# Optimization experiments

Hardware: AMD Instinct MI355X
Metric: run time of the kernel (lower is better)

The kernel has to match this reference:

```python
import jax, jax.numpy as jnp
import numpy as np

N = 100000   # nodes
E = 1600000  # edges
S = 4        # state_dimension
H = 64       # hidden_channels


def _gcn_conv(x, row, col, W, b):
    """PyG GCNConv: h = x @ W; add self-loops; symmetric deg^-1/2 norm; scatter-add; + bias."""
    n = x.shape[0]
    h = x @ W  # [N, out]
    loop = jnp.arange(n, dtype=row.dtype)
    r = jnp.concatenate([row, loop])  # sources (with self-loops)
    c = jnp.concatenate([col, loop])  # targets (with self-loops)
    deg = jax.ops.segment_sum(jnp.ones(r.shape[0], h.dtype), c, num_segments=n)
    dinv = jnp.where(deg > 0, jax.lax.rsqrt(deg), 0.0)
    norm = dinv[r] * dinv[c]                      # [E+N]
    msg = h[r] * norm[:, None]                    # gather + scale, [E+N, out]
    out = jax.ops.segment_sum(msg, c, num_segments=n)  # scatter-add
    return out + b


def setup_inputs() -> dict:
    key = jax.random.key(0)
    k1, k2, k3, k4 = jax.random.split(key, 4)
    x = jax.random.normal(k1, (N, S), dtype=jnp.float32)
    edge_index = jax.random.randint(k2, (2, E), 0, N, dtype=jnp.int32)
    # Glorot-ish init for the two GCNConv linear layers (+ zero bias, PyG default)
    W1 = jax.random.normal(k3, (S, H), dtype=jnp.float32) * (1.0 / np.sqrt(S))
    b1 = jnp.zeros((H,), jnp.float32)
    W2 = jax.random.normal(k4, (H, S), dtype=jnp.float32) * (1.0 / np.sqrt(H))
    b2 = jnp.zeros((S,), jnp.float32)
    return {"x": x, "edge_index": edge_index, "W1": W1, "b1": b1, "W2": W2, "b2": b2}


def reference(x, edge_index, W1, b1, W2, b2):
    row, col = edge_index[0], edge_index[1]
    h = _gcn_conv(x, row, col, W1, b1)
    h = jax.nn.relu(h)
    out = _gcn_conv(h, row, col, W2, b2)
    return out
```

## Files before the change

### kernel.cpp

```cpp
#include <hip/hip_runtime.h>


#define CSHIFT  10
#define CNODES  1024
#define EPB     4096
#define PTH     512
#define PERBLK  96
#define CAPC    18432
#define HCAP    9216
#define ANODES  128
#define ACAP    2432

__global__ void __launch_bounds__(PTH) k_part(
        const int* __restrict__ row, const int* __restrict__ col,
        int e, int Kc, int NB, int* __restrict__ cnt,
        unsigned* __restrict__ stripe) {
    __shared__ int cur[128];
    int t = threadIdx.x, bx = blockIdx.x;
    if (t < 128) cur[t] = 0;
    __syncthreads();
    int lo = bx * EPB;
    int cbuf[8], rbuf[8];
#pragma unroll
    for (int k = 0; k < 8; ++k) {
        int i = lo + t + k * PTH;
        if (i < e) { cbuf[k] = col[i]; rbuf[k] = row[i]; }
        else { cbuf[k] = -1; rbuf[k] = 0; }
    }
    size_t sbase = (size_t)bx * PERBLK;
    size_t bstride = (size_t)NB * PERBLK;
#pragma unroll
    for (int k = 0; k < 8; ++k) {
        int c = cbuf[k];
        if (c < 0) continue;
        int b = c >> CSHIFT;
        int j = atomicAdd(&cur[b], 1);
        if (j < PERBLK)
            stripe[(size_t)b * bstride + sbase + j] =
                ((unsigned)rbuf[k] << CSHIFT) | (unsigned)(c & (CNODES - 1));
    }
    __syncthreads();
    if (t < Kc) cnt[t * NB + bx] = min(cur[t], PERBLK);
}

__global__ void __launch_bounds__(1024) k_sortH(
        const int* __restrict__ cnt, const unsigned* __restrict__ stripe,
        unsigned* __restrict__ sortedg, int* __restrict__ rstart,
        int* __restrict__ mtot, const float4* __restrict__ x,
        float* __restrict__ dinv, float4* __restrict__ y, int n, int NB) {
    __shared__ int hist[CNODES];
    __shared__ int cur[512];
    __shared__ int cntl[512];
    __shared__ unsigned sorted[HCAP];
    __shared__ int wsum[16], wpre[16];
    __shared__ int lowsh, msh;
    int bh = blockIdx.x, b = bh >> 1, h = bh & 1;
    int t = threadIdx.x, lane = t & 63, wv = t >> 6;
    for (int i = t; i < NB; i += 1024) cntl[i] = cnt[b * NB + i];
    hist[t] = 0;
    __syncthreads();
    size_t s0 = (size_t)b * NB * PERBLK;
    int nslot4 = (NB * PERBLK) >> 2;
    const uint4* st4 = (const uint4*)(stripe + s0);
    for (int g = t; g < nslot4; g += 1024) {
        int slot = g << 2;
        int seg = slot / PERBLK;
        int j = slot - seg * PERBLK;
        int cb = cntl[seg];
        if (j >= cb) continue;
        uint4 w = st4[g];
        atomicAdd(&hist[w.x & (CNODES - 1)], 1);
        if (j + 1 < cb) atomicAdd(&hist[w.y & (CNODES - 1)], 1);
        if (j + 2 < cb) atomicAdd(&hist[w.z & (CNODES - 1)], 1);
        if (j + 3 < cb) atomicAdd(&hist[w.w & (CNODES - 1)], 1);
    }
    __syncthreads();
    int hv = hist[t];
    int v = hv;
#pragma unroll
    for (int off = 1; off < 64; off <<= 1) {
        int u = __shfl_up(v, off);
        if (lane >= off) v += u;
    }
    if (lane == 63) wsum[wv] = v;
    __syncthreads();
    if (t < 16) {
        int s = 0;
        for (int i = 0; i < t; ++i) s += wsum[i];
        wpre[t] = s;
    }
    __syncthreads();
    int incl = v + wpre[wv];
    if (t == 511) lowsh = incl;
    if (t == 1023) msh = incl;
    __syncthreads();
    int st = incl - hv;
    int low = lowsh, m = msh;
    int base = h ? low : 0;
    if ((t >> 9) == h) {
        cur[t & 511] = st - base;
        rstart[(b << CSHIFT) + t] = b * CAPC + st;
        int node = (b << CSHIFT) + t;
        if (node < n) {
            float di = rsqrtf((float)hv + 1.0f);
            dinv[node] = di;
            float4 xv = x[node];
            y[node] = make_float4(xv.x * di, xv.y * di, xv.z * di, xv.w * di);
        }
    }
    if (t == 0 && h == 0) mtot[b] = m;
    __syncthreads();
    for (int g = t; g < nslot4; g += 1024) {
        int slot = g << 2;
        int seg = slot / PERBLK;
        int j = slot - seg * PERBLK;
        int cb = cntl[seg];
        if (j >= cb) continue;
        uint4 w = st4[g];
        int l0 = w.x & (CNODES - 1);
        if ((l0 >> 9) == h) { int p = atomicAdd(&cur[l0 & 511], 1); if (p < HCAP) sorted[p] = w.x >> CSHIFT; }
        if (j + 1 < cb) { int l = w.y & (CNODES - 1);
            if ((l >> 9) == h) { int p = atomicAdd(&cur[l & 511], 1); if (p < HCAP) sorted[p] = w.y >> CSHIFT; } }
        if (j + 2 < cb) { int l = w.z & (CNODES - 1);
            if ((l >> 9) == h) { int p = atomicAdd(&cur[l & 511], 1); if (p < HCAP) sorted[p] = w.z >> CSHIFT; } }
        if (j + 3 < cb) { int l = w.w & (CNODES - 1);
            if ((l >> 9) == h) { int p = atomicAdd(&cur[l & 511], 1); if (p < HCAP) sorted[p] = w.w >> CSHIFT; } }
    }
    __syncthreads();
    int cown = h ? (m - low) : low;
    int wb = min(cown, HCAP);
    size_t d0 = (size_t)b * CAPC + base;
    for (int i = t; i < wb; i += 1024) sortedg[d0 + i] = sorted[i];
}

__global__ void __launch_bounds__(512) k_mid(
        const unsigned* __restrict__ ere, const int* __restrict__ rstart,
        const int* __restrict__ mtot, const float* __restrict__ dinv,
        const float4* __restrict__ x, const float4* __restrict__ y,
        const float* __restrict__ W1, const float* __restrict__ b1,
        const float* __restrict__ W2, const float* __restrict__ b2,
        float4* __restrict__ z, float4* __restrict__ out, int n) {
    __shared__ unsigned recs[ACAP];
    __shared__ float4 sums[ANODES];
    int g = blockIdx.x, t = threadIdx.x;
    int nlo = g * ANODES;
    int b = nlo >> CSHIFT;
    int s0 = rstart[nlo];
    int e0 = ((g & 7) == 7) ? b * CAPC + min(mtot[b], CAPC)
                            : rstart[nlo + ANODES];
    int len = min(e0 - s0, ACAP);
    for (int i = t; i < len; i += 512) recs[i] = ere[s0 + i];
    __syncthreads();
    int tt = t >> 2, q = t & 3;
    int s = rstart[nlo + tt] - s0;
    int epos = (tt == ANODES - 1) ? len : min(rstart[nlo + tt + 1] - s0, len);
    float vx = 0.f, vy = 0.f, vz = 0.f, vw = 0.f;
    int i = s + q;
    while (i + 12 < epos) {
        int r0 = recs[i], r1 = recs[i + 4], r2 = recs[i + 8], r3 = recs[i + 12];
        float4 a0 = y[r0], a1 = y[r1], a2 = y[r2], a3 = y[r3];
        vx += a0.x + a1.x + a2.x + a3.x;
        vy += a0.y + a1.y + a2.y + a3.y;
        vz += a0.z + a1.z + a2.z + a3.z;
        vw += a0.w + a1.w + a2.w + a3.w;
        i += 16;
    }
    for (; i < epos; i += 4) {
        float4 a = y[recs[i]];
        vx += a.x; vy += a.y; vz += a.z; vw += a.w;
    }
    vx += __shfl_xor(vx, 1); vx += __shfl_xor(vx, 2);
    vy += __shfl_xor(vy, 1); vy += __shfl_xor(vy, 2);
    vz += __shfl_xor(vz, 1); vz += __shfl_xor(vz, 2);
    vw += __shfl_xor(vw, 1); vw += __shfl_xor(vw, 2);
    if (q == 0) sums[tt] = make_float4(vx, vy, vz, vw);
    __syncthreads();
    int node = nlo + t;
    if (t < ANODES && node < n) {
        float di = dinv[node], sl = di * di;
        float4 sv = sums[t];
        float4 xv = x[node];
        float a0 = di * sv.x + xv.x * sl;
        float a1 = di * sv.y + xv.y * sl;
        float a2 = di * sv.z + xv.z * sl;
        float a3 = di * sv.w + xv.w * sl;
        float t0 = 0.f, t1 = 0.f, t2 = 0.f, t3 = 0.f;
#pragma unroll 8
        for (int j = 0; j < 64; ++j) {
            float hh = b1[j] + a0 * W1[j] + a1 * W1[64 + j] + a2 * W1[128 + j] + a3 * W1[192 + j];
            hh = fmaxf(hh, 0.f);
            t0 += hh * W2[j * 4 + 0];
            t1 += hh * W2[j * 4 + 1];
            t2 += hh * W2[j * 4 + 2];
            t3 += hh * W2[j * 4 + 3];
        }
        z[node] = make_float4(t0 * di, t1 * di, t2 * di, t3 * di);
        out[node] = make_float4(b2[0] + t0 * sl, b2[1] + t1 * sl,
                                b2[2] + t2 * sl, b2[3] + t3 * sl);
    }
}

__global__ void __launch_bounds__(512) k_acc2(
        const unsigned* __restrict__ ere, const int* __restrict__ rstart,
        const int* __restrict__ mtot, const float* __restrict__ dinv,
        const float4* __restrict__ z, float4* __restrict__ out, int n) {
    __shared__ unsigned recs[ACAP];
    __shared__ float4 sums[ANODES];
    int g = blockIdx.x, t = threadIdx.x;
    int nlo = g * ANODES;
    int b = nlo >> CSHIFT;
    int s0 = rstart[nlo];
    int e0 = ((g & 7) == 7) ? b * CAPC + min(mtot[b], CAPC)
                            : rstart[nlo + ANODES];
    int len = min(e0 - s0, ACAP);
    for (int i = t; i < len; i += 512) recs[i] = ere[s0 + i];
    __syncthreads();
    int tt = t >> 2, q = t & 3;
    int s = rstart[nlo + tt] - s0;
    int epos = (tt == ANODES - 1) ? len : min(rstart[nlo + tt + 1] - s0, len);
    float vx = 0.f, vy = 0.f, vz = 0.f, vw = 0.f;
    int i = s + q;
    while (i + 12 < epos) {
        int r0 = recs[i], r1 = recs[i + 4], r2 = recs[i + 8], r3 = recs[i + 12];
        float4 a0 = z[r0], a1 = z[r1], a2 = z[r2], a3 = z[r3];
        vx += a0.x + a1.x + a2.x + a3.x;
        vy += a0.y + a1.y + a2.y + a3.y;
        vz += a0.z + a1.z + a2.z + a3.z;
        vw += a0.w + a1.w + a2.w + a3.w;
        i += 16;
    }
    for (; i < epos; i += 4) {
        float4 a = z[recs[i]];
        vx += a.x; vy += a.y; vz += a.z; vw += a.w;
    }
    vx += __shfl_xor(vx, 1); vx += __shfl_xor(vx, 2);
    vy += __shfl_xor(vy, 1); vy += __shfl_xor(vy, 2);
    vz += __shfl_xor(vz, 1); vz += __shfl_xor(vz, 2);
    vw += __shfl_xor(vw, 1); vw += __shfl_xor(vw, 2);
    if (q == 0) sums[tt] = make_float4(vx, vy, vz, vw);
    __syncthreads();
    int node = nlo + t;
    if (t < ANODES && node < n) {
        float di = dinv[node];
        float4 sv = sums[t];
        float4 o = out[node];
        out[node] = make_float4(o.x + di * sv.x, o.y + di * sv.y,
                                o.z + di * sv.z, o.w + di * sv.w);
    }
}

extern "C" void kernel_launch(void* const* d_in, const int* in_sizes, int n_in,
                              void* d_out, int out_size, void* d_ws, size_t ws_size,
                              hipStream_t stream) {
    const float* x  = (const float*)d_in[0];
    const int* edge = (const int*)d_in[1];
    const float* W1 = (const float*)d_in[2];
    const float* b1 = (const float*)d_in[3];
    const float* W2 = (const float*)d_in[4];
    const float* b2 = (const float*)d_in[5];
    float* out = (float*)d_out;

    const int n = in_sizes[0] / 4;
    const int e = in_sizes[1] / 2;
    const int* row = edge;
    const int* col = edge + e;
    const int Kc = (n + CNODES - 1) >> CSHIFT;
    const int NB = (e + EPB - 1) / EPB;

    char* ws = (char*)d_ws;
    float* y    = (float*)ws;  ws += (size_t)4 * n * 4;
    float* zmid = (float*)ws;  ws += (size_t)4 * n * 4;
    float* dinv = (float*)ws;  ws += (size_t)n * 4;
    unsigned* stripe = (unsigned*)ws;  ws += (size_t)Kc * NB * PERBLK * 4;
    unsigned* sortedg = (unsigned*)ws; ws += (size_t)Kc * CAPC * 4;
    int* cnt    = (int*)ws;    ws += (size_t)Kc * NB * 4;
    int* rstart = (int*)ws;    ws += (size_t)Kc * CNODES * 4;
    int* mtot   = (int*)ws;    ws += (size_t)Kc * 4;

    const int ga = (n + ANODES - 1) / ANODES;

    k_part<<<NB, PTH, 0, stream>>>(row, col, e, Kc, NB, cnt, stripe);
    k_sortH<<<2 * Kc, 1024, 0, stream>>>(cnt, stripe, sortedg, rstart, mtot,
                                         (const float4*)x, dinv, (float4*)y,
                                         n, NB);
    k_mid<<<ga, 512, 0, stream>>>(sortedg, rstart, mtot, dinv, (const float4*)x,
                                  (const float4*)y, W1, b1, W2, b2,
                                  (float4*)zmid, (float4*)out, n);
    k_acc2<<<ga, 512, 0, stream>>>(sortedg, rstart, mtot, dinv,
                                   (const float4*)zmid, (float4*)out, n);
}
```

Measured before the change: 124.0 us.

## Compute degrees with global atomics and split the per-node MLP across lanes

Node degrees are now counted with global atomicAdd in the partition kernel. This removes the first full pass over the stripe buffer that the sort kernel used to build its shared-memory histogram. The per-node MLP in k_mid is spread over 4 lanes, each handling 16 hidden units, with weights staged in shared memory (padded W2) and a shuffle reduction; this replaces 128 threads each looping over 64 units with global weight reads. Both aggregation kernels also drop the shared sums buffer and its __syncthreads. The costs are 1.6M global atomics, an extra memset, and degrees that count all edges even if a stripe overflows its cap.

Measured after the change: 182.5 us. +47.1%, slower.

```diff
diff --git a/kernel.cpp b/kernel.cpp
--- a/kernel.cpp
+++ b/kernel.cpp
@@ -14,7 +14,7 @@
 __global__ void __launch_bounds__(PTH) k_part(
         const int* __restrict__ row, const int* __restrict__ col,
         int e, int Kc, int NB, int* __restrict__ cnt,
-        unsigned* __restrict__ stripe) {
+        unsigned* __restrict__ stripe, int* __restrict__ deg) {
     __shared__ int cur[128];
     int t = threadIdx.x, bx = blockIdx.x;
     if (t < 128) cur[t] = 0;
@@ -38,6 +38,7 @@
         if (j < PERBLK)
             stripe[(size_t)b * bstride + sbase + j] =
                 ((unsigned)rbuf[k] << CSHIFT) | (unsigned)(c & (CNODES - 1));
+        atomicAdd(&deg[c], 1);
     }
     __syncthreads();
     if (t < Kc) cnt[t * NB + bx] = min(cur[t], PERBLK);
@@ -45,10 +46,10 @@
 
 __global__ void __launch_bounds__(1024) k_sortH(
         const int* __restrict__ cnt, const unsigned* __restrict__ stripe,
+        const int* __restrict__ deg,
         unsigned* __restrict__ sortedg, int* __restrict__ rstart,
         int* __restrict__ mtot, const float4* __restrict__ x,
         float* __restrict__ dinv, float4* __restrict__ y, int n, int NB) {
-    __shared__ int hist[CNODES];
     __shared__ int cur[512];
     __shared__ int cntl[512];
     __shared__ unsigned sorted[HCAP];
@@ -57,25 +58,8 @@
     int bh = blockIdx.x, b = bh >> 1, h = bh & 1;
     int t = threadIdx.x, lane = t & 63, wv = t >> 6;
     for (int i = t; i < NB; i += 1024) cntl[i] = cnt[b * NB + i];
-    hist[t] = 0;
-    __syncthreads();
-    size_t s0 = (size_t)b * NB * PERBLK;
-    int nslot4 = (NB * PERBLK) >> 2;
-    const uint4* st4 = (const uint4*)(stripe + s0);
-    for (int g = t; g < nslot4; g += 1024) {
-        int slot = g << 2;
-        int seg = slot / PERBLK;
-        int j = slot - seg * PERBLK;
-        int cb = cntl[seg];
-        if (j >= cb) continue;
-        uint4 w = st4[g];
-        atomicAdd(&hist[w.x & (CNODES - 1)], 1);
-        if (j + 1 < cb) atomicAdd(&hist[w.y & (CNODES - 1)], 1);
-        if (j + 2 < cb) atomicAdd(&hist[w.z & (CNODES - 1)], 1);
-        if (j + 3 < cb) atomicAdd(&hist[w.w & (CNODES - 1)], 1);
-    }
-    __syncthreads();
-    int hv = hist[t];
+    int node = (b << CSHIFT) + t;
+    int hv = (node < n) ? deg[node] : 0;
     int v = hv;
 #pragma unroll
     for (int off = 1; off < 64; off <<= 1) {
@@ -100,7 +84,6 @@
     if ((t >> 9) == h) {
         cur[t & 511] = st - base;
         rstart[(b << CSHIFT) + t] = b * CAPC + st;
-        int node = (b << CSHIFT) + t;
         if (node < n) {
             float di = rsqrtf((float)hv + 1.0f);
             dinv[node] = di;
@@ -110,6 +93,9 @@
     }
     if (t == 0 && h == 0) mtot[b] = m;
     __syncthreads();
+    size_t s0 = (size_t)b * NB * PERBLK;
+    int nslot4 = (NB * PERBLK) >> 2;
+    const uint4* st4 = (const uint4*)(stripe + s0);
     for (int g = t; g < nslot4; g += 1024) {
         int slot = g << 2;
         int seg = slot / PERBLK;
@@ -141,7 +127,10 @@
         const float* __restrict__ W2, const float* __restrict__ b2,
         float4* __restrict__ z, float4* __restrict__ out, int n) {
     __shared__ unsigned recs[ACAP];
-    __shared__ float4 sums[ANODES];
+    __shared__ float sW1[256];
+    __shared__ float sW2[320];
+    __shared__ float sb1[64];
+    __shared__ float sb2[4];
     int g = blockIdx.x, t = threadIdx.x;
     int nlo = g * ANODES;
     int b = nlo >> CSHIFT;
@@ -150,6 +139,11 @@
                             : rstart[nlo + ANODES];
     int len = min(e0 - s0, ACAP);
     for (int i = t; i < len; i += 512) recs[i] = ere[s0 + i];
+    if (t < 256) {
+        sW1[t] = W1[t];
+        sW2[(t >> 2) * 5 + (t & 3)] = W2[t];
+    } else if (t < 320) sb1[t - 256] = b1[t - 256];
+    else if (t < 324) sb2[t - 320] = b2[t - 320];
     __syncthreads();
     int tt = t >> 2, q = t & 3;
     int s = rstart[nlo + tt] - s0;
@@ -173,30 +167,36 @@
     vy += __shfl_xor(vy, 1); vy += __shfl_xor(vy, 2);
     vz += __shfl_xor(vz, 1); vz += __shfl_xor(vz, 2);
     vw += __shfl_xor(vw, 1); vw += __shfl_xor(vw, 2);
-    if (q == 0) sums[tt] = make_float4(vx, vy, vz, vw);
-    __syncthreads();
-    int node = nlo + t;
-    if (t < ANODES && node < n) {
+    int node = nlo + tt;
+    if (node < n) {
         float di = dinv[node], sl = di * di;
-        float4 sv = sums[t];
         float4 xv = x[node];
-        float a0 = di * sv.x + xv.x * sl;
-        float a1 = di * sv.y + xv.y * sl;
-        float a2 = di * sv.z + xv.z * sl;
-        float a3 = di * sv.w + xv.w * sl;
+        float a0 = di * vx + xv.x * sl;
+        float a1 = di * vy + xv.y * sl;
+        float a2 = di * vz + xv.z * sl;
+        float a3 = di * vw + xv.w * sl;
         float t0 = 0.f, t1 = 0.f, t2 = 0.f, t3 = 0.f;
-#pragma unroll 8
-        for (int j = 0; j < 64; ++j) {
-            float hh = b1[j] + a0 * W1[j] + a1 * W1[64 + j] + a2 * W1[128 + j] + a3 * W1[192 + j];
+        int j0 = q << 4;
+#pragma unroll
+        for (int k = 0; k < 16; ++k) {
+            int j = j0 + k;
+            float hh = sb1[j] + a0 * sW1[j] + a1 * sW1[64 + j]
+                     + a2 * sW1[128 + j] + a3 * sW1[192 + j];
             hh = fmaxf(hh, 0.f);
-            t0 += hh * W2[j * 4 + 0];
-            t1 += hh * W2[j * 4 + 1];
-            t2 += hh * W2[j * 4 + 2];
-            t3 += hh * W2[j * 4 + 3];
+            t0 += hh * sW2[j * 5 + 0];
+            t1 += hh * sW2[j * 5 + 1];
+            t2 += hh * sW2[j * 5 + 2];
+            t3 += hh * sW2[j * 5 + 3];
         }
-        z[node] = make_float4(t0 * di, t1 * di, t2 * di, t3 * di);
-        out[node] = make_float4(b2[0] + t0 * sl, b2[1] + t1 * sl,
-                                b2[2] + t2 * sl, b2[3] + t3 * sl);
+        t0 += __shfl_xor(t0, 1); t0 += __shfl_xor(t0, 2);
+        t1 += __shfl_xor(t1, 1); t1 += __shfl_xor(t1, 2);
+        t2 += __shfl_xor(t2, 1); t2 += __shfl_xor(t2, 2);
+        t3 += __shfl_xor(t3, 1); t3 += __shfl_xor(t3, 2);
+        if (q == 0) {
+            z[node] = make_float4(t0 * di, t1 * di, t2 * di, t3 * di);
+            out[node] = make_float4(sb2[0] + t0 * sl, sb2[1] + t1 * sl,
+                                    sb2[2] + t2 * sl, sb2[3] + t3 * sl);
+        }
     }
 }
 
@@ -205,7 +205,6 @@
         const int* __restrict__ mtot, const float* __restrict__ dinv,
         const float4* __restrict__ z, float4* __restrict__ out, int n) {
     __shared__ unsigned recs[ACAP];
-    __shared__ float4 sums[ANODES];
     int g = blockIdx.x, t = threadIdx.x;
     int nlo = g * ANODES;
     int b = nlo >> CSHIFT;
@@ -237,15 +236,12 @@
     vy += __shfl_xor(vy, 1); vy += __shfl_xor(vy, 2);
     vz += __shfl_xor(vz, 1); vz += __shfl_xor(vz, 2);
     vw += __shfl_xor(vw, 1); vw += __shfl_xor(vw, 2);
-    if (q == 0) sums[tt] = make_float4(vx, vy, vz, vw);
-    __syncthreads();
-    int node = nlo + t;
-    if (t < ANODES && node < n) {
+    int node = nlo + tt;
+    if (q == 0 && node < n) {
         float di = dinv[node];
-        float4 sv = sums[t];
         float4 o = out[node];
-        out[node] = make_float4(o.x + di * sv.x, o.y + di * sv.y,
-                                o.z + di * sv.z, o.w + di * sv.w);
+        out[node] = make_float4(o.x + di * vx, o.y + di * vy,
+                                o.z + di * vz, o.w + di * vw);
     }
 }
 
@@ -276,13 +272,15 @@
     int* cnt    = (int*)ws;    ws += (size_t)Kc * NB * 4;
     int* rstart = (int*)ws;    ws += (size_t)Kc * CNODES * 4;
     int* mtot   = (int*)ws;    ws += (size_t)Kc * 4;
+    int* deg    = (int*)ws;    ws += (size_t)n * 4;
 
     const int ga = (n + ANODES - 1) / ANODES;
 
-    k_part<<<NB, PTH, 0, stream>>>(row, col, e, Kc, NB, cnt, stripe);
-    k_sortH<<<2 * Kc, 1024, 0, stream>>>(cnt, stripe, sortedg, rstart, mtot,
-                                         (const float4*)x, dinv, (float4*)y,
-                                         n, NB);
+    hipMemsetAsync(deg, 0, (size_t)n * 4, stream);
+    k_part<<<NB, PTH, 0, stream>>>(row, col, e, Kc, NB, cnt, stripe, deg);
+    k_sortH<<<2 * Kc, 1024, 0, stream>>>(cnt, stripe, deg, sortedg, rstart,
+                                         mtot, (const float4*)x, dinv,
+                                         (float4*)y, n, NB);
     k_mid<<<ga, 512, 0, stream>>>(sortedg, rstart, mtot, dinv, (const float4*)x,
                                   (const float4*)y, W1, b1, W2, b2,
                                   (float4*)zmid, (float4*)out, n);
```
